# Kernel tuning notes

Hardware: AMD Instinct MI355X
Metric: run time of the kernel (lower is better)

Reference implementation:

```python
import jax, jax.numpy as jnp
import numpy as np

B = 128  # batch


def _genperm(key, n):
    k1, k2 = jax.random.split(key)
    perm = jax.random.permutation(k1, n).astype(jnp.int32)
    scale = jax.random.uniform(k2, (n,), jnp.float32, 0.5, 2.0)
    return perm, scale


def _enc(x, p, s):  # y = A x with A[i, p[i]] = s[i]  (generalized permutation)
    return s * x[..., p]


def _dec(y, p, s):  # x = A^{-1} y
    return (y / s)[..., jnp.argsort(p)]


def _kconv(y, pin, sin, pout, sout, w, b, chw, stride):
    C, H, W = chw
    x = _dec(y, pin, sin)[:, :-1].reshape(-1, C, H, W)  # drop homogeneous 1
    pad = (w.shape[-1] - 1) // 2
    out = jax.lax.conv_general_dilated(x, w, (stride, stride), [(pad, pad), (pad, pad)],
                                       dimension_numbers=('NCHW', 'OIHW', 'NCHW'))
    out = out + b[None, :, None, None]
    flat = out.reshape(out.shape[0], -1)
    flat = jnp.concatenate([flat, jnp.ones((flat.shape[0], 1), flat.dtype)], axis=1)
    return _enc(flat, pout, sout)


def _krelu(y, pa, sa, pb, sb):  # B * relu(A^{-1} y); relu(1)=1 preserves homogeneous elt
    return _enc(jax.nn.relu(_dec(y, pa, sa)), pb, sb)


def _klin(y, pin, sin, pout, sout, W, b):
    x = _dec(y, pin, sin)[:, :-1]
    out = x @ W.T + b
    out = jnp.concatenate([out, jnp.ones((out.shape[0], 1), out.dtype)], axis=1)
    return _enc(out, pout, sout)


def setup_inputs():
    key = jax.random.key(0)
    ks = iter(jax.random.split(key, 64))
    d = {}
    N = {'0': 3 * 32 * 32 + 1, '1': 96 * 32 * 32 + 1, '3': 96 * 16 * 16 + 1,
         '4': 192 * 16 * 16 + 1, '6': 192 * 8 * 8 + 1, '9': 10 * 8 * 8 + 1,
         '10': 101, '11': 11}
    for name, n in [('0', N['0']), ('1a', N['1']), ('1b', N['1']), ('3a', N['3']),
                    ('3b', N['3']), ('4a', N['4']), ('4b', N['4']), ('6a', N['6']),
                    ('6b', N['6']), ('9a', N['9']), ('9b', N['9']), ('10a', N['10']),
                    ('10b', N['10']), ('11', N['11'])]:
        p, s = _genperm(next(ks), n)
        d['p' + name] = p
        d['s' + name] = s
    convs = [('1', (96, 3, 3, 3)), ('2', (96, 96, 3, 3)), ('3', (96, 96, 3, 3)),
             ('4', (192, 96, 3, 3)), ('5', (192, 192, 3, 3)), ('6', (192, 192, 3, 3)),
             ('7', (192, 192, 3, 3)), ('8', (192, 192, 1, 1)), ('9', (10, 192, 1, 1))]
    for name, shp in convs:
        fan_in = float(np.prod(shp[1:]))
        d['w' + name] = jax.random.normal(next(ks), shp, jnp.float32) / np.sqrt(fan_in)
        d['b' + name] = 0.01 * jax.random.normal(next(ks), (shp[0],), jnp.float32)
    d['fw1'] = jax.random.normal(next(ks), (100, 640), jnp.float32) / np.sqrt(640.0)
    d['fb1'] = 0.01 * jax.random.normal(next(ks), (100,), jnp.float32)
    d['fw2'] = jax.random.normal(next(ks), (10, 100), jnp.float32) / np.sqrt(100.0)
    d['fb2'] = 0.01 * jax.random.normal(next(ks), (10,), jnp.float32)
    x0 = jax.random.normal(next(ks), (B, 3 * 32 * 32), jnp.float32)
    x0h = jnp.concatenate([x0, jnp.ones((B, 1), jnp.float32)], axis=1)
    d['A0x0_affine'] = _enc(x0h, d['p0'], d['s0'])
    return d


def reference(A0x0_affine, w1, b1, w2, b2, w3, b3, w4, b4, w5, b5, w6, b6, w7, b7,
              w8, b8, w9, b9, fw1, fb1, fw2, fb2,
              p0, s0, p1a, s1a, p1b, s1b, p3a, s3a, p3b, s3b, p4a, s4a, p4b, s4b,
              p6a, s6a, p6b, s6b, p9a, s9a, p9b, s9b, p10a, s10a, p10b, s10b, p11, s11):
    y = _kconv(A0x0_affine, p0, s0, p1a, s1a, w1, b1, (3, 32, 32), 1)
    y = _krelu(y, p1a, s1a, p1b, s1b)                     # relu1
    y = _kconv(y, p1b, s1b, p1a, s1a, w2, b2, (96, 32, 32), 1)
    y = _krelu(y, p1a, s1a, p1b, s1b)                     # relu1 (reused)
    y = _kconv(y, p1b, s1b, p3a, s3a, w3, b3, (96, 32, 32), 2)   # conv3 (bn fused)
    y = _krelu(y, p3a, s3a, p3b, s3b)                     # relu3
    y = _kconv(y, p3b, s3b, p4a, s4a, w4, b4, (96, 16, 16), 1)
    y = _krelu(y, p4a, s4a, p4b, s4b)                     # relu4
    y = _kconv(y, p4b, s4b, p4a, s4a, w5, b5, (192, 16, 16), 1)
    y = _krelu(y, p4a, s4a, p4b, s4b)                     # relu4 (reused)
    y = _kconv(y, p4b, s4b, p6a, s6a, w6, b6, (192, 16, 16), 2)  # conv6 (bn fused)
    y = _krelu(y, p6a, s6a, p6b, s6b)                     # relu6
    y = _kconv(y, p6b, s6b, p6a, s6a, w7, b7, (192, 8, 8), 1)
    y = _krelu(y, p6a, s6a, p6b, s6b)                     # relu6 (reused)
    y = _kconv(y, p6b, s6b, p6a, s6a, w8, b8, (192, 8, 8), 1)
    y = _krelu(y, p6a, s6a, p6b, s6b)                     # relu6 (reused)
    y = _kconv(y, p6b, s6b, p9a, s9a, w9, b9, (192, 8, 8), 1)
    y = _krelu(y, p9a, s9a, p9b, s9b)                     # relu9
    y = _klin(y, p9b, s9b, p10a, s10a, fw1, fb1)          # fc1
    y = _krelu(y, p10a, s10a, p10b, s10b)                 # relu10
    y = _klin(y, p10b, s10b, p11, s11, fw2, fb2)          # fc2
    return y  # keyed output, shape (B, 11)
```

## Files before the change

### kernel.cpp

```cpp
#include <hip/hip_runtime.h>
#include <hip/hip_bf16.h>

#define BATCH 128
#define CDIV(a, b) (((a) + (b) - 1) / (b))

typedef __attribute__((ext_vector_type(8))) short short8;
typedef __attribute__((ext_vector_type(4))) float f32x4;

template <int V> struct ic { static constexpr int value = V; };
template <int... I> struct iseq {};
template <int N, int... I> struct mkseq : mkseq<N - 1, N - 1, I...> {};
template <int... I> struct mkseq<0, I...> { using type = iseq<I...>; };
template <class F, int... I>
__device__ __forceinline__ void unroll_all(F&& f, iseq<I...>) { (f(ic<I>{}), ...); }

__device__ __forceinline__ void gload_lds16(const void* g, void* l) {
    __builtin_amdgcn_global_load_lds(
        (const __attribute__((address_space(1))) void*)g,
        (__attribute__((address_space(3))) void*)l, 16, 0, 0);
}

__global__ void fill0_f32(float* __restrict__ p, int n) {
    int i = blockIdx.x * blockDim.x + threadIdx.x;
    if (i < n) p[i] = 0.0f;
}

__global__ void decode_kernel(const float* __restrict__ y, const int* __restrict__ p,
                              const float* __restrict__ s, float* __restrict__ x) {
    const int n = 3073;
    int idx = blockIdx.x * blockDim.x + threadIdx.x;
    if (idx >= BATCH * n) return;
    int i = idx % n, b = idx / n;
    int pi = p[i];
    if (pi >= 3072) return;
    float v = y[(size_t)b * n + i] / s[i];
    int c = pi >> 10; int r = pi & 1023; int h = r >> 5; int w = r & 31;
    x[((size_t)(b * 34 + h + 1) * 34 + (w + 1)) * 4 + c] = v;
}

struct HaloDesc { __hip_bfloat16* p; int Hp, Wp, C; };
struct Halo4 { HaloDesc d[4]; int cum[5]; int n; };

__global__ void halo_zero_multi(Halo4 h) {
    int idx = blockIdx.x * 256 + threadIdx.x;
    if (idx >= h.cum[h.n]) return;
    int seg = 0;
    while (idx >= h.cum[seg + 1]) ++seg;
    int local = idx - h.cum[seg];
    HaloDesc d = h.d[seg];
    int perB = (2 * d.Wp + 2 * (d.Hp - 2)) * d.C / 8;
    int b = local / perB;
    int r = (local % perB) * 8;
    int WpC = d.Wp * d.C;
    long addr;
    if (r < WpC) {
        addr = (long)(b * d.Hp) * WpC + r;
    } else if (r < 2 * WpC) {
        addr = (long)(b * d.Hp + d.Hp - 1) * WpC + (r - WpC);
    } else {
        int r3 = r - 2 * WpC;
        int sideN = (d.Hp - 2) * d.C;
        int side = r3 / sideN;
        int r4 = r3 % sideN;
        int row = 1 + r4 / d.C, c = r4 % d.C;
        addr = ((long)(b * d.Hp + row) * d.Wp + (side ? d.Wp - 1 : 0)) * d.C + c;
    }
    *(uint4*)((char*)d.p + addr * 2) = uint4{0, 0, 0, 0};
}

struct WtSeg { const float* src; __hip_bfloat16* dst; int Cout, Cin, KK, CoutPad; };
struct Wt8 { WtSeg s[8]; int cum[9]; };

__global__ void wt_transform_multi(Wt8 w) {
    int idx = blockIdx.x * 256 + threadIdx.x;
    if (idx >= w.cum[8]) return;
    int seg = 0;
    while (idx >= w.cum[seg + 1]) ++seg;
    int local = idx - w.cum[seg];
    WtSeg sg = w.s[seg];
    int c2 = local % 32; int t = local / 32;
    int co = t % sg.CoutPad; int t2 = t / sg.CoutPad;
    int KS = sg.Cin / 32;
    int kk = t2 % KS; int pos = t2 / KS;
    int cin = kk * 32 + c2;
    float v = (co < sg.Cout) ? sg.src[((size_t)co * sg.Cin + cin) * sg.KK + pos] : 0.0f;
    sg.dst[local] = __float2bfloat16(v);
}

__global__ __launch_bounds__(256) void conv1_kernel(
    const float* __restrict__ in, const float* __restrict__ w,
    const float* __restrict__ bias, __hip_bfloat16* __restrict__ out) {
    __shared__ float ws[96 * 27];
    __shared__ float bs[96];
    for (int i = threadIdx.x; i < 96 * 27; i += 256) ws[i] = w[i];
    if (threadIdx.x < 96) bs[threadIdx.x] = bias[threadIdx.x];
    __syncthreads();
    int idx = blockIdx.x * 256 + threadIdx.x;
    int q = idx & 3; int pix = idx >> 2;
    int b = pix >> 10, r = pix & 1023, oh = r >> 5, ow = r & 31;
    const float* ib = in + ((size_t)(b * 34 + oh) * 34 + ow) * 4;
    float patch[9][3];
#pragma unroll
    for (int ph = 0; ph < 3; ++ph)
#pragma unroll
        for (int pw = 0; pw < 3; ++pw) {
            float4 v = *(const float4*)(ib + ((size_t)ph * 34 + pw) * 4);
            patch[ph * 3 + pw][0] = v.x; patch[ph * 3 + pw][1] = v.y; patch[ph * 3 + pw][2] = v.z;
        }
    const int c0 = q * 24;
    float acc[24];
#pragma unroll
    for (int j = 0; j < 24; ++j) acc[j] = bs[c0 + j];
    for (int j = 0; j < 24; ++j) {
        const float* wc = &ws[(c0 + j) * 27];
#pragma unroll
        for (int ci = 0; ci < 3; ++ci)
#pragma unroll
            for (int pos = 0; pos < 9; ++pos)
                acc[j] = fmaf(patch[pos][ci], wc[ci * 9 + pos], acc[j]);
    }
    __hip_bfloat16* ob = out + ((size_t)(b * 34 + oh + 1) * 34 + ow + 1) * 96 + c0;
#pragma unroll
    for (int g = 0; g < 3; ++g) {
        union { uint4 u; unsigned short s[8]; } pk;
#pragma unroll
        for (int e = 0; e < 8; ++e) {
            __hip_bfloat16 hv = __float2bfloat16(fmaxf(acc[g * 8 + e], 0.0f));
            pk.s[e] = *(unsigned short*)&hv;
        }
        *(uint4*)(ob + g * 8) = pk.u;
    }
}

template <int CIN, int COUT, int HIN, int WIN, int STRIDE, int R,
          int WN, int MT, int NTW, int LA, int DEPTH, int THREADS, int MINW>
__global__ __launch_bounds__(THREADS, MINW) void conv_pipe(
    const __hip_bfloat16* __restrict__ in,
    const __hip_bfloat16* __restrict__ wt,
    const float* __restrict__ bias,
    __hip_bfloat16* __restrict__ out) {
    constexpr int HOUT = HIN / STRIDE, WOUT = WIN / STRIDE;
    constexpr int Hp = HIN + 2, Wp = WIN + 2;
    constexpr int Hpo = HOUT + 2, Wpo = WOUT + 2;
    constexpr int D = 2 * R + 1;
    constexpr int KS = CIN / 32;
    constexpr int NSTEP = D * D * KS;
    constexpr int WAVES = THREADS / 64;
    static_assert(WAVES == WN, "one wave row");
    constexpr int BM = MT * 16;
    constexpr int BN = WN * NTW * 16;
    static_assert(BN == COUT, "block covers full N");
    static_assert(BM % WOUT == 0, "whole output rows");
    static_assert(LA >= 3 && DEPTH >= 3 && DEPTH >= LA - 1, "pipeline depth");
    constexpr int BMR = BM / WOUT;
    constexpr int SUPR = (BMR - 1) * STRIDE + D;
    constexpr int CINU = CIN / 8;
    constexpr int UPP = CINU + 1;
    constexpr int ROWU = Wp * CINU;
    constexpr int TOTU = SUPR * ROWU;

    __shared__ short8 ldsA[SUPR * Wp * UPP];
    __shared__ short8 ldsB[WAVES * DEPTH * NTW * 64];

    int wid = threadIdx.x >> 6;
    int lane = threadIdx.x & 63;
    int col = lane & 15, kgrp = lane >> 4;
    int n0 = wid * (NTW * 16);
    int su = col * 4 + kgrp;

    auto issueChunk = [&](int c, int slot) {
        const __hip_bfloat16* src = wt + ((size_t)c * COUT + n0) * 32 + lane * 8;
#pragma unroll
        for (int nt = 0; nt < NTW; ++nt)
            gload_lds16(src + nt * (16 * 32),
                        &ldsB[((wid * DEPTH + slot) * NTW + nt) * 64]);
    };

#pragma unroll
    for (int c = 0; c < LA; ++c)
        if (c < NSTEP) issueChunk(c, c % DEPTH);

    int m0 = blockIdx.x * BM;
    int gor = m0 / WOUT;
    int b = gor / HOUT;
    int oh0 = gor % HOUT;
    int r0 = oh0 * STRIDE + (1 - R);
    const __hip_bfloat16* gsrc = in + ((size_t)(b * Hp + r0) * Wp) * CIN;
    for (int g = threadIdx.x; g < TOTU; g += THREADS) {
        int row = g / ROWU;
        int ur = g - row * ROWU;
        int pix = ur / CINU;
        int c = ur - pix * CINU;
        ldsA[(row * Wp + pix) * UPP + c] = *reinterpret_cast<const short8*>(gsrc + (size_t)g * 8);
    }
    __syncthreads();

    int abaseu[MT];
#pragma unroll
    for (int mt = 0; mt < MT; ++mt) {
        int mloc = mt * 16 + col;
        int orow = mloc / WOUT, ocol = mloc % WOUT;
        abaseu[mt] = ((orow * STRIDE) * Wp + ocol * STRIDE + (1 - R)) * UPP + kgrp;
    }

    short8 af[3][MT], bf[3][NTW];
    f32x4 acc[MT][NTW] = {};

    auto readFrags = [&](int s, auto rIC) {
        constexpr int r = decltype(rIC)::value;
        int pos = s / KS, kk = s - (s / KS) * KS;
        int poff = ((pos / D) * Wp + (pos % D)) * UPP;
#pragma unroll
        for (int mt = 0; mt < MT; ++mt)
            af[r][mt] = ldsA[abaseu[mt] + poff + kk * 4];
        int slot = s % DEPTH;
#pragma unroll
        for (int nt = 0; nt < NTW; ++nt)
            bf[r][nt] = ldsB[((wid * DEPTH + slot) * NTW + nt) * 64 + su];
    };

    readFrags(0, ic<0>{});
    if (1 < NSTEP) readFrags(1, ic<1>{});

    unroll_all([&](auto sc) {
        constexpr int s = decltype(sc)::value;
        if constexpr (s + LA < NSTEP) issueChunk(s + LA, (s + LA) % DEPTH);
        if constexpr (s + 2 < NSTEP) {
            constexpr int I = (s + LA < NSTEP - 1) ? (s + LA) : (NSTEP - 1);
            constexpr int NW0 = (I - (s + 2)) * NTW;
            constexpr int NW = NW0 < 0 ? 0 : NW0;
            asm volatile("s_waitcnt vmcnt(%0)" :: "i"(NW) : "memory");
            readFrags(s + 2, ic<(s + 2) % 3>{});
        }
#pragma unroll
        for (int nt = 0; nt < NTW; ++nt)
#pragma unroll
            for (int mt = 0; mt < MT; ++mt)
                acc[mt][nt] = __builtin_amdgcn_mfma_f32_16x16x32_bf16(
                    af[s % 3][mt], bf[s % 3][nt], acc[mt][nt], 0, 0, 0);
    }, typename mkseq<NSTEP>::type{});

#pragma unroll
    for (int mt = 0; mt < MT; ++mt) {
#pragma unroll
        for (int nt = 0; nt < NTW; ++nt) {
            int cout = n0 + nt * 16 + col;
            float bv = bias[cout];
#pragma unroll
            for (int rg = 0; rg < 4; ++rg) {
                int mloc = mt * 16 + kgrp * 4 + rg;
                int orow = mloc / WOUT, ocol = mloc % WOUT;
                float v = fmaxf(acc[mt][nt][rg] + bv, 0.0f);
                out[((size_t)(b * Hpo + oh0 + orow + 1) * Wpo + ocol + 1) * COUT + cout] =
                    __float2bfloat16(v);
            }
        }
    }
}

template <int CIN, int COUT, int HIN, int WIN, int STRIDE, int R,
          int WM, int WN, int MT, int NTW, int PW, int THREADS, int MINW>
__global__ __launch_bounds__(THREADS, MINW) void conv_lds(
    const __hip_bfloat16* __restrict__ in,
    const __hip_bfloat16* __restrict__ wt,
    const float* __restrict__ bias,
    __hip_bfloat16* __restrict__ out) {
    constexpr int HOUT = HIN / STRIDE, WOUT = WIN / STRIDE;
    constexpr int Hp = HIN + 2, Wp = WIN + 2;
    constexpr int Hpo = HOUT + 2, Wpo = WOUT + 2;
    constexpr int D = 2 * R + 1;
    constexpr int KS = CIN / 32;
    constexpr int NSTEP = D * D * KS;
    constexpr int BM = WM * MT * 16;
    constexpr int BN = WN * NTW * 16;
    static_assert(BN == COUT, "block covers full N");
    static_assert(BM % WOUT == 0, "block tile = whole output rows");
    static_assert(THREADS / 64 == WM * WN, "wave count");
    constexpr int BMR = BM / WOUT;
    constexpr int SUPR = (BMR - 1) * STRIDE + D;
    constexpr int CINU = CIN / 8;
    constexpr int UPP = CINU + 1;
    constexpr int ROWU = Wp * CINU;
    constexpr int TOTU = SUPR * ROWU;

    __shared__ short8 lds[SUPR * Wp * UPP];

    int m0 = blockIdx.x * BM;
    int gor = m0 / WOUT;
    int b = gor / HOUT;
    int oh0 = gor % HOUT;
    int r0 = oh0 * STRIDE + (1 - R);

    const __hip_bfloat16* gsrc = in + ((size_t)(b * Hp + r0) * Wp) * CIN;
    for (int g = threadIdx.x; g < TOTU; g += THREADS) {
        int row = g / ROWU;
        int ur = g - row * ROWU;
        int pix = ur / CINU;
        int c = ur - pix * CINU;
        lds[(row * Wp + pix) * UPP + c] = *reinterpret_cast<const short8*>(gsrc + (size_t)g * 8);
    }
    __syncthreads();

    int wid = threadIdx.x >> 6;
    int lane = threadIdx.x & 63;
    int col = lane & 15, kgrp = lane >> 4;
    int wm = wid / WN, wn = wid % WN;
    int n0 = wn * NTW * 16;

    int apix[MT];
#pragma unroll
    for (int mt = 0; mt < MT; ++mt) {
        int mloc = (wm * MT + mt) * 16 + col;
        int orow = mloc / WOUT, ocol = mloc % WOUT;
        apix[mt] = (orow * STRIDE) * Wp + ocol * STRIDE + (1 - R);
    }
    const __hip_bfloat16* bbase[NTW];
#pragma unroll
    for (int nt = 0; nt < NTW; ++nt)
        bbase[nt] = wt + (size_t)(n0 + nt * 16 + col) * 32 + kgrp * 8;

    short8 abuf[3][MT];
    short8 bbuf[PW][NTW];
    f32x4 acc[MT][NTW] = {};

    auto ldA = [&](int s, int slot) {
        int pos = s / KS, kk = s - (s / KS) * KS;
        int dh = pos / D, dw = pos - dh * D;
        int poff = dh * Wp + dw;
#pragma unroll
        for (int mt = 0; mt < MT; ++mt)
            abuf[slot][mt] = lds[(apix[mt] + poff) * UPP + kk * 4 + kgrp];
    };
    auto ldB = [&](int s, int slot) {
        size_t off = (size_t)s * (COUT * 32);
#pragma unroll
        for (int nt = 0; nt < NTW; ++nt)
            bbuf[slot][nt] = *reinterpret_cast<const short8*>(bbase[nt] + off);
    };

#pragma unroll
    for (int s = 0; s < PW - 1; ++s)
        if (s < NSTEP) ldB(s, s);
    ldA(0, 0);
    if (1 < NSTEP) ldA(1, 1);
    __builtin_amdgcn_sched_barrier(0);

#pragma unroll
    for (int s = 0; s < NSTEP; ++s) {
        if (s + PW - 1 < NSTEP) ldB(s + PW - 1, (s + PW - 1) % PW);
        if (s + 2 < NSTEP) ldA(s + 2, (s + 2) % 3);
        __builtin_amdgcn_sched_barrier(0);
#pragma unroll
        for (int nt = 0; nt < NTW; ++nt)
#pragma unroll
            for (int mt = 0; mt < MT; ++mt)
                acc[mt][nt] = __builtin_amdgcn_mfma_f32_16x16x32_bf16(
                    abuf[s % 3][mt], bbuf[s % PW][nt], acc[mt][nt], 0, 0, 0);
    }

#pragma unroll
    for (int mt = 0; mt < MT; ++mt) {
#pragma unroll
        for (int nt = 0; nt < NTW; ++nt) {
            int cout = n0 + nt * 16 + col;
            float bv = bias[cout];
#pragma unroll
            for (int rg = 0; rg < 4; ++rg) {
                int mloc = (wm * MT + mt) * 16 + kgrp * 4 + rg;
                int orow = mloc / WOUT, ocol = mloc % WOUT;
                float v = fmaxf(acc[mt][nt][rg] + bv, 0.0f);
                out[((size_t)(b * Hpo + oh0 + orow + 1) * Wpo + ocol + 1) * COUT + cout] =
                    __float2bfloat16(v);
            }
        }
    }
}

__global__ __launch_bounds__(256) void conv9_kernel(
    const __hip_bfloat16* __restrict__ in, const __hip_bfloat16* __restrict__ wt,
    const float* __restrict__ bias, float* __restrict__ out) {
    int wid = threadIdx.x >> 6;
    int lane = threadIdx.x & 63;
    int wave = blockIdx.x * 4 + wid;
    int m0 = wave * 16;
    int col = lane & 15;
    int kgrp = lane >> 4;
    int m = m0 + col;
    int b = m >> 6; int r = m & 63; int oh = r >> 3; int ow = r & 7;
    const __hip_bfloat16* abase = in + ((size_t)(b * 10 + oh + 1) * 10 + ow + 1) * 192 + kgrp * 8;
    f32x4 acc = {};
#pragma unroll
    for (int kk = 0; kk < 6; ++kk) {
        short8 bfr = *reinterpret_cast<const short8*>(wt + ((size_t)kk * 16 + col) * 32 + kgrp * 8);
        short8 a = *reinterpret_cast<const short8*>(abase + kk * 32);
        acc = __builtin_amdgcn_mfma_f32_16x16x32_bf16(a, bfr, acc, 0, 0, 0);
    }
    if (col < 10) {
        float bv = bias[col];
#pragma unroll
        for (int rg = 0; rg < 4; ++rg) {
            int m2 = m0 + kgrp * 4 + rg;
            int b2 = m2 >> 6; int r2 = m2 & 63;
            out[(size_t)b2 * 640 + col * 64 + r2] = fmaxf(acc[rg] + bv, 0.0f);
        }
    }
}

__global__ __launch_bounds__(128) void head_kernel(
    const float* __restrict__ act9, const float* __restrict__ fw1, const float* __restrict__ fb1,
    const float* __restrict__ fw2, const float* __restrict__ fb2,
    const int* __restrict__ p11, const float* __restrict__ s11, float* __restrict__ out) {
    __shared__ float x[640];
    __shared__ float h[100];
    __shared__ float o[10];
    int b = blockIdx.x, t = threadIdx.x;
    for (int i = t; i < 160; i += 128)
        ((float4*)x)[i] = ((const float4*)(act9 + (size_t)b * 640))[i];
    __syncthreads();
    if (t < 100) {
        float acc = fb1[t];
        const float4* wr = (const float4*)(fw1 + (size_t)t * 640);
        const float4* xv = (const float4*)x;
#pragma unroll 4
        for (int i = 0; i < 160; ++i) {
            float4 wv = wr[i], qv = xv[i];
            acc = fmaf(wv.x, qv.x, acc); acc = fmaf(wv.y, qv.y, acc);
            acc = fmaf(wv.z, qv.z, acc); acc = fmaf(wv.w, qv.w, acc);
        }
        h[t] = fmaxf(acc, 0.0f);
    }
    __syncthreads();
    if (t < 10) {
        float acc = fb2[t];
        for (int i = 0; i < 100; ++i) acc = fmaf(h[i], fw2[t * 100 + i], acc);
        o[t] = acc;
    }
    __syncthreads();
    if (t < 11) {
        int pi = p11[t];
        out[(size_t)b * 11 + t] = s11[t] * (pi == 10 ? 1.0f : o[pi]);
    }
}

extern "C" void kernel_launch(void* const* d_in, const int* in_sizes, int n_in,
                              void* d_out, int out_size, void* d_ws, size_t ws_size,
                              hipStream_t stream) {
    const int*   p0  = (const int*)  d_in[0];
    const float* s0  = (const float*)d_in[1];
    const int*   p11 = (const int*)  d_in[26];
    const float* s11 = (const float*)d_in[27];
    const float* w1 = (const float*)d_in[28]; const float* b1 = (const float*)d_in[29];
    const float* w2 = (const float*)d_in[30]; const float* b2 = (const float*)d_in[31];
    const float* w3 = (const float*)d_in[32]; const float* b3 = (const float*)d_in[33];
    const float* w4 = (const float*)d_in[34]; const float* b4 = (const float*)d_in[35];
    const float* w5 = (const float*)d_in[36]; const float* b5 = (const float*)d_in[37];
    const float* w6 = (const float*)d_in[38]; const float* b6 = (const float*)d_in[39];
    const float* w7 = (const float*)d_in[40]; const float* b7 = (const float*)d_in[41];
    const float* w8 = (const float*)d_in[42]; const float* b8 = (const float*)d_in[43];
    const float* w9 = (const float*)d_in[44]; const float* b9 = (const float*)d_in[45];
    const float* fw1 = (const float*)d_in[46]; const float* fb1 = (const float*)d_in[47];
    const float* fw2 = (const float*)d_in[48]; const float* fb2 = (const float*)d_in[49];
    const float* A0 = (const float*)d_in[50];
    float* out = (float*)d_out;

    size_t off = 0;
    auto alloc = [&](size_t bytes) {
        void* p = (char*)d_ws + off;
        off += (bytes + 255) & ~(size_t)255;
        return p;
    };
    const size_t SZ_3434_96  = (size_t)BATCH * 34 * 34 * 96 * 2;
    const size_t SZ_1818_96  = (size_t)BATCH * 18 * 18 * 96 * 2;
    const size_t SZ_1818_192 = (size_t)BATCH * 18 * 18 * 192 * 2;

    float* dec = (float*)alloc((size_t)BATCH * 34 * 34 * 4 * 4);
    __hip_bfloat16* regA = (__hip_bfloat16*)alloc(SZ_3434_96);
    __hip_bfloat16* regB = (__hip_bfloat16*)alloc(SZ_3434_96);
    __hip_bfloat16* regC = (__hip_bfloat16*)alloc(SZ_1818_96);
    __hip_bfloat16* regD = (__hip_bfloat16*)alloc(SZ_1818_192);
    __hip_bfloat16* wt2 = (__hip_bfloat16*)alloc((size_t)9 * 96 * 96 * 2);
    __hip_bfloat16* wt3 = (__hip_bfloat16*)alloc((size_t)9 * 96 * 96 * 2);
    __hip_bfloat16* wt4 = (__hip_bfloat16*)alloc((size_t)9 * 192 * 96 * 2);
    __hip_bfloat16* wt5 = (__hip_bfloat16*)alloc((size_t)9 * 192 * 192 * 2);
    __hip_bfloat16* wt6 = (__hip_bfloat16*)alloc((size_t)9 * 192 * 192 * 2);
    __hip_bfloat16* wt7 = (__hip_bfloat16*)alloc((size_t)9 * 192 * 192 * 2);
    __hip_bfloat16* wt8 = (__hip_bfloat16*)alloc((size_t)1 * 192 * 192 * 2);
    __hip_bfloat16* wt9 = (__hip_bfloat16*)alloc((size_t)16 * 192 * 2);
    float* act9 = (float*)alloc((size_t)BATCH * 640 * 4);

    const int TPB = 256;

    int decN = BATCH * 34 * 34 * 4;
    fill0_f32<<<CDIV(decN, TPB), TPB, 0, stream>>>(dec, decN);
    decode_kernel<<<CDIV(BATCH * 3073, TPB), TPB, 0, stream>>>(A0, p0, s0, dec);

    Wt8 wts;
    wts.s[0] = {w2, wt2, 96, 96, 9, 96};
    wts.s[1] = {w3, wt3, 96, 96, 9, 96};
    wts.s[2] = {w4, wt4, 192, 96, 9, 192};
    wts.s[3] = {w5, wt5, 192, 192, 9, 192};
    wts.s[4] = {w6, wt6, 192, 192, 9, 192};
    wts.s[5] = {w7, wt7, 192, 192, 9, 192};
    wts.s[6] = {w8, wt8, 192, 192, 1, 192};
    wts.s[7] = {w9, wt9, 10, 192, 1, 16};
    wts.cum[0] = 0;
    for (int i = 0; i < 8; ++i)
        wts.cum[i + 1] = wts.cum[i] + wts.s[i].KK * wts.s[i].CoutPad * wts.s[i].Cin;
    wt_transform_multi<<<CDIV(wts.cum[8], TPB), TPB, 0, stream>>>(wts);

    auto chunks = [](int Hp, int Wp, int C) { return BATCH * (2 * Wp + 2 * (Hp - 2)) * C / 8; };
    Halo4 h0;
    h0.d[0] = {regA, 34, 34, 96};
    h0.d[1] = {regB, 34, 34, 96};
    h0.d[2] = {regC, 18, 18, 96};
    h0.d[3] = {regD, 18, 18, 192};
    h0.n = 4; h0.cum[0] = 0;
    for (int i = 0; i < 4; ++i)
        h0.cum[i + 1] = h0.cum[i] + chunks(h0.d[i].Hp, h0.d[i].Wp, h0.d[i].C);
    halo_zero_multi<<<CDIV(h0.cum[4], TPB), TPB, 0, stream>>>(h0);

    conv1_kernel<<<2048, 256, 0, stream>>>(dec, w1, b1, regA);
    conv_pipe<96, 96, 32, 32, 1, 1, 2, 4, 3, 4, 4, 128, 2><<<2048, 128, 0, stream>>>(regA, wt2, b2, regB);
    Halo4 h5; h5.d[0] = {regA, 18, 18, 192}; h5.n = 1;
    h5.cum[0] = 0; h5.cum[1] = chunks(18, 18, 192);
    halo_zero_multi<<<CDIV(h5.cum[1], TPB), TPB, 0, stream>>>(h5);
    conv_pipe<96, 96, 32, 32, 2, 1, 2, 2, 3, 4, 4, 128, 2><<<1024, 128, 0, stream>>>(regB, wt3, b3, regC);
    conv_pipe<96, 192, 16, 16, 1, 1, 4, 4, 3, 4, 4, 256, 2><<<512, 256, 0, stream>>>(regC, wt4, b4, regD);
    Halo4 h6; h6.d[0] = {regC, 10, 10, 192}; h6.n = 1;
    h6.cum[0] = 0; h6.cum[1] = chunks(10, 10, 192);
    halo_zero_multi<<<CDIV(h6.cum[1], TPB), TPB, 0, stream>>>(h6);
    conv_pipe<192, 192, 16, 16, 1, 1, 4, 4, 3, 3, 3, 256, 2><<<512, 256, 0, stream>>>(regD, wt5, b5, regA);
    conv_pipe<192, 192, 16, 16, 2, 1, 4, 1, 3, 3, 3, 256, 2><<<512, 256, 0, stream>>>(regA, wt6, b6, regC);
    conv_pipe<192, 192, 8, 8, 1, 1, 4, 2, 3, 4, 4, 256, 2><<<256, 256, 0, stream>>>(regC, wt7, b7, regD);
    conv_lds<192, 192, 8, 8, 1, 0, 1, 4, 1, 3, 6, 256, 3><<<512, 256, 0, stream>>>(regD, wt8, b8, regB);
    conv9_kernel<<<128, 256, 0, stream>>>(regB, wt9, b9, act9);
    head_kernel<<<BATCH, 128, 0, stream>>>(act9, fw1, fb1, fw2, fb2, p11, s11, out);
}
```

Before: 207.2 us.

## Add double-buffered implicit-GEMM conv kernel and use it for conv2-conv5

```diff
diff --git a/kernel.cpp b/kernel.cpp
--- a/kernel.cpp
+++ b/kernel.cpp
@@ -133,6 +133,123 @@
 }
 
 template <int CIN, int COUT, int HIN, int WIN, int STRIDE, int R,
+          int BMPIX, int WM, int WN, int THREADS, int MINW>
+__global__ __launch_bounds__(THREADS, MINW) void conv_gemm(
+    const __hip_bfloat16* __restrict__ in,
+    const __hip_bfloat16* __restrict__ wt,
+    const float* __restrict__ bias,
+    __hip_bfloat16* __restrict__ out) {
+    constexpr int HOUT = HIN / STRIDE, WOUT = WIN / STRIDE;
+    constexpr int Hp = HIN + 2, Wp = WIN + 2;
+    constexpr int Hpo = HOUT + 2, Wpo = WOUT + 2;
+    constexpr int D = 2 * R + 1;
+    constexpr int KS = CIN / 32;
+    constexpr int NSTEP = D * D * KS;
+    constexpr int WAVES = THREADS / 64;
+    static_assert(WAVES == WM * WN, "wave grid");
+    constexpr int MT = BMPIX / WM / 16;
+    constexpr int NTW = COUT / WN / 16;
+    constexpr int AU = BMPIX * 4;
+    constexpr int BU = COUT * 4;
+    constexpr int APW = AU / WAVES;
+    static_assert(APW % 64 == 0, "A stage divides");
+    constexpr int AG = APW / 64;
+    constexpr int BPW = BU / WAVES;
+    constexpr int BG = BPW / 64;
+    constexpr int BREM = BPW % 64;
+
+    __shared__ short8 ldsA[2 * AU];
+    __shared__ short8 ldsB[2 * BU];
+
+    int wid = threadIdx.x >> 6;
+    int lane = threadIdx.x & 63;
+    int col = lane & 15, kgrp = lane >> 4;
+    int wm = wid / WN, wn = wid % WN;
+    int n0 = wn * (NTW * 16);
+
+    const __hip_bfloat16* aSrc[AG];
+#pragma unroll
+    for (int i = 0; i < AG; ++i) {
+        int u = wid * APW + i * 64 + lane;
+        int p = u >> 2, q = u & 3;
+        int gp = blockIdx.x * BMPIX + p;
+        int b = gp / (HOUT * WOUT);
+        int r = gp % (HOUT * WOUT);
+        int oh = r / WOUT, ow = r % WOUT;
+        aSrc[i] = in + ((size_t)(b * Hp + oh * STRIDE + 1 - R) * Wp + ow * STRIDE + 1 - R) * CIN + q * 8;
+    }
+    int bOff[BG + 1];
+#pragma unroll
+    for (int i = 0; i < BG + (BREM ? 1 : 0); ++i) {
+        int u = wid * BPW + i * 64 + lane;
+        bOff[i] = (u >> 2) * 32 + (u & 3) * 8;
+    }
+
+    auto stage = [&](int aoff, size_t woff, int buf) {
+#pragma unroll
+        for (int i = 0; i < AG; ++i)
+            gload_lds16(aSrc[i] + aoff, &ldsA[buf * AU + wid * APW + i * 64]);
+#pragma unroll
+        for (int i = 0; i < BG; ++i)
+            gload_lds16(wt + woff + bOff[i], &ldsB[buf * BU + wid * BPW + i * 64]);
+        if constexpr (BREM > 0) {
+            if (lane < BREM)
+                gload_lds16(wt + woff + bOff[BG], &ldsB[buf * BU + wid * BPW + BG * 64]);
+        }
+    };
+    auto stepA = [](int s) {
+        int pos = s / KS, kk = s - (s / KS) * KS;
+        return ((pos / D) * Wp + (pos % D)) * CIN + kk * 32;
+    };
+
+    f32x4 acc[MT][NTW] = {};
+
+    stage(stepA(0), 0, 0);
+    __syncthreads();
+
+    unroll_all([&](auto sc) {
+        constexpr int s = decltype(sc)::value;
+        if constexpr (s + 1 < NSTEP)
+            stage(stepA(s + 1), (size_t)(s + 1) * (COUT * 32), (s + 1) & 1);
+        constexpr int buf = s & 1;
+        short8 af[MT], bf[NTW];
+#pragma unroll
+        for (int mt = 0; mt < MT; ++mt)
+            af[mt] = ldsA[buf * AU + (wm * MT * 16 + mt * 16 + col) * 4 + kgrp];
+#pragma unroll
+        for (int nt = 0; nt < NTW; ++nt)
+            bf[nt] = ldsB[buf * BU + (n0 + nt * 16 + col) * 4 + kgrp];
+#pragma unroll
+        for (int nt = 0; nt < NTW; ++nt)
+#pragma unroll
+            for (int mt = 0; mt < MT; ++mt)
+                acc[mt][nt] = __builtin_amdgcn_mfma_f32_16x16x32_bf16(
+                    af[mt], bf[nt], acc[mt][nt], 0, 0, 0);
+        __syncthreads();
+    }, typename mkseq<NSTEP>::type{});
+
+#pragma unroll
+    for (int mt = 0; mt < MT; ++mt) {
+#pragma unroll
+        for (int nt = 0; nt < NTW; ++nt) {
+            int cout = n0 + nt * 16 + col;
+            float bv = bias[cout];
+#pragma unroll
+            for (int rg = 0; rg < 4; ++rg) {
+                int p = wm * MT * 16 + mt * 16 + kgrp * 4 + rg;
+                int gp = blockIdx.x * BMPIX + p;
+                int b = gp / (HOUT * WOUT);
+                int r = gp % (HOUT * WOUT);
+                int oh = r / WOUT, ow = r % WOUT;
+                float v = fmaxf(acc[mt][nt][rg] + bv, 0.0f);
+                out[((size_t)(b * Hpo + oh + 1) * Wpo + ow + 1) * COUT + cout] =
+                    __float2bfloat16(v);
+            }
+        }
+    }
+}
+
+template <int CIN, int COUT, int HIN, int WIN, int STRIDE, int R,
           int WN, int MT, int NTW, int LA, int DEPTH, int THREADS, int MINW>
 __global__ __launch_bounds__(THREADS, MINW) void conv_pipe(
     const __hip_bfloat16* __restrict__ in,
@@ -151,7 +268,6 @@
     constexpr int BN = WN * NTW * 16;
     static_assert(BN == COUT, "block covers full N");
     static_assert(BM % WOUT == 0, "whole output rows");
-    static_assert(LA >= 3 && DEPTH >= 3 && DEPTH >= LA - 1, "pipeline depth");
     constexpr int BMR = BM / WOUT;
     constexpr int SUPR = (BMR - 1) * STRIDE + D;
     constexpr int CINU = CIN / 8;
@@ -520,16 +636,16 @@
     halo_zero_multi<<<CDIV(h0.cum[4], TPB), TPB, 0, stream>>>(h0);
 
     conv1_kernel<<<2048, 256, 0, stream>>>(dec, w1, b1, regA);
-    conv_pipe<96, 96, 32, 32, 1, 1, 2, 4, 3, 4, 4, 128, 2><<<2048, 128, 0, stream>>>(regA, wt2, b2, regB);
+    conv_gemm<96, 96, 32, 32, 1, 1, 128, 2, 2, 256, 3><<<1024, 256, 0, stream>>>(regA, wt2, b2, regB);
     Halo4 h5; h5.d[0] = {regA, 18, 18, 192}; h5.n = 1;
     h5.cum[0] = 0; h5.cum[1] = chunks(18, 18, 192);
     halo_zero_multi<<<CDIV(h5.cum[1], TPB), TPB, 0, stream>>>(h5);
-    conv_pipe<96, 96, 32, 32, 2, 1, 2, 2, 3, 4, 4, 128, 2><<<1024, 128, 0, stream>>>(regB, wt3, b3, regC);
-    conv_pipe<96, 192, 16, 16, 1, 1, 4, 4, 3, 4, 4, 256, 2><<<512, 256, 0, stream>>>(regC, wt4, b4, regD);
+    conv_gemm<96, 96, 32, 32, 2, 1, 64, 2, 2, 256, 3><<<512, 256, 0, stream>>>(regB, wt3, b3, regC);
+    conv_gemm<96, 192, 16, 16, 1, 1, 64, 1, 4, 256, 3><<<512, 256, 0, stream>>>(regC, wt4, b4, regD);
     Halo4 h6; h6.d[0] = {regC, 10, 10, 192}; h6.n = 1;
     h6.cum[0] = 0; h6.cum[1] = chunks(10, 10, 192);
     halo_zero_multi<<<CDIV(h6.cum[1], TPB), TPB, 0, stream>>>(h6);
-    conv_pipe<192, 192, 16, 16, 1, 1, 4, 4, 3, 3, 3, 256, 2><<<512, 256, 0, stream>>>(regD, wt5, b5, regA);
+    conv_gemm<192, 192, 16, 16, 1, 1, 64, 1, 4, 256, 3><<<512, 256, 0, stream>>>(regD, wt5, b5, regA);
     conv_pipe<192, 192, 16, 16, 2, 1, 4, 1, 3, 3, 3, 256, 2><<<512, 256, 0, stream>>>(regA, wt6, b6, regC);
     conv_pipe<192, 192, 8, 8, 1, 1, 4, 2, 3, 4, 4, 256, 2><<<256, 256, 0, stream>>>(regC, wt7, b7, regD);
     conv_lds<192, 192, 8, 8, 1, 0, 1, 4, 1, 3, 6, 256, 3><<<512, 256, 0, stream>>>(regD, wt8, b8, regB);
```

Measured after the change: 218.8 us. 5.6% more time.
